# Kernel optimization log

Measured on AMD Instinct MI355X. Metric: run time of the kernel, lower is better.

## Reference

```python
import jax, jax.numpy as jnp
import numpy as np

N_NODES = 20000
EPS_BN = 1e-5
NEG_SLOPE = 0.2


def gat_conv(x, W, att_src, att_dst, bias, src, dst, heads, out_ch, concat):
    n = x.shape[0]
    h = (x @ W).reshape(n, heads, out_ch)                       # [N,H,C]
    a_src = jnp.sum(h * att_src, axis=-1)                       # [N,H]
    a_dst = jnp.sum(h * att_dst, axis=-1)                       # [N,H]
    e = jax.nn.leaky_relu(a_src[src] + a_dst[dst], NEG_SLOPE)   # [E,H]
    # segment softmax over incoming edges of each destination node
    m = jax.ops.segment_max(e, dst, num_segments=n)             # [N,H]
    e = jnp.exp(e - m[dst])
    denom = jax.ops.segment_sum(e, dst, num_segments=n)         # [N,H]
    alpha = e / (denom[dst] + 1e-16)                            # [E,H]
    msg = alpha[:, :, None] * h[src]                            # [E,H,C]
    out = jax.ops.segment_sum(msg, dst, num_segments=n)         # [N,H,C]
    if concat:
        out = out.reshape(n, heads * out_ch)
    else:
        out = out.mean(axis=1)
    return out + bias


def batch_norm(x, gamma, beta):
    mu = x.mean(axis=0)
    var = x.var(axis=0)  # biased, matches torch normalization
    return (x - mu) * jax.lax.rsqrt(var + EPS_BN) * gamma + beta


def setup_inputs() -> dict:
    key = jax.random.key(0)
    ks = jax.random.split(key, 16)
    n, d_in, hid, heads = N_NODES, 768, 128, 8
    n_edges = 160000
    x = jax.random.normal(ks[0], (n, d_in), dtype=jnp.float32)
    edge_index = jax.random.randint(ks[1], (2, n_edges), 0, n, dtype=jnp.int64)
    s = lambda fi, fo: (2.0 / (fi + fo)) ** 0.5
    return {
        "x": x,
        "edge_index": edge_index,
        "W1": jax.random.normal(ks[2], (d_in, heads * hid), jnp.float32) * s(d_in, heads * hid),
        "att_src1": jax.random.normal(ks[3], (heads, hid), jnp.float32) * 0.1,
        "att_dst1": jax.random.normal(ks[4], (heads, hid), jnp.float32) * 0.1,
        "bias1": jnp.zeros((heads * hid,), jnp.float32),
        "bn1_g": jnp.ones((heads * hid,), jnp.float32),
        "bn1_b": jnp.zeros((heads * hid,), jnp.float32),
        "W2": jax.random.normal(ks[5], (heads * hid, hid), jnp.float32) * s(heads * hid, hid),
        "att_src2": jax.random.normal(ks[6], (1, hid), jnp.float32) * 0.1,
        "att_dst2": jax.random.normal(ks[7], (1, hid), jnp.float32) * 0.1,
        "bias2": jnp.zeros((hid,), jnp.float32),
        "bn2_g": jnp.ones((hid,), jnp.float32),
        "bn2_b": jnp.zeros((hid,), jnp.float32),
        "Wc1": jax.random.normal(ks[8], (hid, 64), jnp.float32) * s(hid, 64),
        "bc1": jnp.zeros((64,), jnp.float32),
        "Wc2": jax.random.normal(ks[9], (64, 2), jnp.float32) * s(64, 2),
        "bc2": jnp.zeros((2,), jnp.float32),
    }


def reference(x, edge_index, W1, att_src1, att_dst1, bias1, bn1_g, bn1_b,
              W2, att_src2, att_dst2, bias2, bn2_g, bn2_b,
              Wc1, bc1, Wc2, bc2):
    n = x.shape[0]
    # PyG GATConv default: add self-loops
    loops = jnp.arange(n, dtype=edge_index.dtype)
    src = jnp.concatenate([edge_index[0], loops])
    dst = jnp.concatenate([edge_index[1], loops])

    h = gat_conv(x, W1, att_src1, att_dst1, bias1, src, dst, heads=8, out_ch=128, concat=True)
    h = jax.nn.elu(batch_norm(h, bn1_g, bn1_b))
    # dropout disabled (deterministic reference)
    h = gat_conv(h, W2, att_src2, att_dst2, bias2, src, dst, heads=1, out_ch=128, concat=False)
    h = jax.nn.elu(batch_norm(h, bn2_g, bn2_b))
    h = jax.nn.elu(h @ Wc1 + bc1)
    return h @ Wc2 + bc2  # [N, 2] logits
```

## Files before the change

kernel.cpp:

```cpp
#include <hip/hip_runtime.h>
#include <stdint.h>

typedef unsigned short u16;
typedef __bf16 bf16x8 __attribute__((ext_vector_type(8)));
typedef float f32x4 __attribute__((ext_vector_type(4)));

__device__ __forceinline__ float b2f(u16 u) {
    unsigned x = ((unsigned)u) << 16;
    return __builtin_bit_cast(float, x);
}
__device__ __forceinline__ u16 f2b(float f) {
    unsigned x = __builtin_bit_cast(unsigned, f);
    x = x + 0x7fffu + ((x >> 16) & 1u);
    return (u16)(x >> 16);
}
__device__ __forceinline__ float leaky(float v) { return v > 0.f ? v : 0.2f * v; }
__device__ __forceinline__ float elu(float v) { return v > 0.f ? v : expm1f(v); }

__device__ __forceinline__ void gload16(const u16* g, u16* l) {
    __builtin_amdgcn_global_load_lds((const __attribute__((address_space(1))) void*)(const void*)g,
                                     (__attribute__((address_space(3))) void*)(void*)l, 16, 0, 0);
}

__global__ void k_pre(const float* __restrict__ x, u16* __restrict__ xb,
                      const float* __restrict__ W1, u16* __restrict__ w1t,
                      const float* __restrict__ W2, u16* __restrict__ w2t,
                      const int* __restrict__ ei, int* __restrict__ flag,
                      int* __restrict__ deg, size_t n4, int E0, int N) {
    int bid = blockIdx.x, t = threadIdx.x;
    if (bid < 2048) {
        size_t i = (size_t)bid * 256 + t;
        const size_t stride = (size_t)2048 * 256;
        for (size_t k = i; k < n4; k += stride) {
            float4 v = ((const float4*)x)[k];
            ushort4 o;
            o.x = f2b(v.x); o.y = f2b(v.y); o.z = f2b(v.z); o.w = f2b(v.w);
            ((ushort4*)xb)[k] = o;
        }
        for (size_t k = i; k < (size_t)N; k += stride) deg[k] = 0;
        if (bid == 0) {
            if (t == 0) *flag = 0;
            __syncthreads();
            int lim = E0 < 4096 ? E0 : 4096;
            int any = 0;
            for (int k = t; k < lim; k += 256) any |= (ei[2 * k + 1] != 0);
            if (any) atomicOr(flag, 1);
        }
    } else {
        __shared__ float tile[32][33];
        int b = bid - 2048;
        const float* in; u16* outp; int R, C, cx, ry;
        if (b < 768) { in = W1; outp = w1t; R = 768; C = 1024; cx = b & 31; ry = b >> 5; }
        else { int b2 = b - 768; in = W2; outp = w2t; R = 1024; C = 128; cx = b2 & 3; ry = b2 >> 2; }
        int tx = t & 31, ty = t >> 5;
        int c0 = cx * 32, r0 = ry * 32;
        #pragma unroll
        for (int i = 0; i < 32; i += 8)
            tile[ty + i][tx] = in[(size_t)(r0 + ty + i) * C + c0 + tx];
        __syncthreads();
        #pragma unroll
        for (int i = 0; i < 32; i += 8)
            outp[(size_t)(c0 + ty + i) * R + r0 + tx] = f2b(tile[tx][ty + i]);
    }
}

#define GBM 128
#define GBN 128
#define GBK 64
#define LDT 72
#define SPLITK 4

__global__ __launch_bounds__(256) void k_gemm(const u16* __restrict__ A, const u16* __restrict__ Bt,
                                              u16* __restrict__ C, int M, int NN, int K, int nCB) {
    __shared__ __align__(16) u16 As[GBM][GBK];
    __shared__ __align__(16) u16 Bs[GBN][GBK];
    int nwg = gridDim.x, orig = blockIdx.x;
    int q = nwg >> 3, r8 = nwg & 7, xcd = orig & 7, sub = orig >> 3;
    int wgid = (xcd < r8 ? xcd * (q + 1) : r8 * (q + 1) + (xcd - r8) * q) + sub;
    int rb = wgid / nCB, cb = wgid % nCB;
    int brow = rb * GBM, bcol = cb * GBN;

    int t = threadIdx.x, lane = t & 63, wid = t >> 6;
    int wm = (wid >> 1) * 64, wn = (wid & 1) * 64;
    int fr = lane & 15, fq = lane >> 4;
    f32x4 acc[4][4] = {};
    int srow = lane >> 3;
    int scol = (((lane & 7) ^ srow)) * 8;
    int dcol = (lane & 7) * 8;
    int nK = K / GBK;
    for (int kt = 0; kt < nK; ++kt) {
        int k0 = kt * GBK;
        #pragma unroll
        for (int cc = 0; cc < 8; ++cc) {
            int c = wid * 8 + cc;
            int r = (c & 15) * 8 + srow;
            if (c < 16) gload16(A + (size_t)(brow + r) * K + k0 + scol, &As[r][dcol]);
            else        gload16(Bt + (size_t)(bcol + r) * K + k0 + scol, &Bs[r][dcol]);
        }
        __syncthreads();
        #pragma unroll
        for (int kk = 0; kk < 2; ++kk) {
            int ko = kk * 32 + fq * 8;
            int kos = ko ^ ((fr & 7) << 3);
            bf16x8 af[4], bg[4];
            #pragma unroll
            for (int i = 0; i < 4; ++i) {
                af[i] = *reinterpret_cast<const bf16x8*>(&As[wm + i * 16 + fr][kos]);
                bg[i] = *reinterpret_cast<const bf16x8*>(&Bs[wn + i * 16 + fr][kos]);
            }
            #pragma unroll
            for (int mi = 0; mi < 4; ++mi)
                #pragma unroll
                for (int ni = 0; ni < 4; ++ni)
                    acc[mi][ni] = __builtin_amdgcn_mfma_f32_16x16x32_bf16(af[mi], bg[ni], acc[mi][ni], 0, 0, 0);
        }
        __syncthreads();
    }
    #pragma unroll
    for (int mi = 0; mi < 4; ++mi) {
        #pragma unroll
        for (int j = 0; j < 4; ++j) {
            int row = brow + wm + mi * 16 + fq * 4 + j;
            if (row < M) {
                #pragma unroll
                for (int ni = 0; ni < 4; ++ni) {
                    int col = bcol + wn + ni * 16 + fr;
                    C[(size_t)row * NN + col] = f2b(acc[mi][ni][j]);
                }
            }
        }
    }
}

__global__ __launch_bounds__(256) void k_gemm2(const u16* __restrict__ A, const u16* __restrict__ Bt,
                                               float* __restrict__ Cp, int M, int K,
                                               const float* __restrict__ scA, const float* __restrict__ shA) {
    __shared__ __align__(16) u16 As[GBM][LDT];
    __shared__ __align__(16) u16 Bs[GBN][LDT];
    int brow = blockIdx.x * GBM;
    int ks = blockIdx.y;
    int kBase = ks * (K / SPLITK);
    int t = threadIdx.x;
    int lane = t & 63, wid = t >> 6;
    int wm = (wid >> 1) * 64, wn = (wid & 1) * 64;
    int fr = lane & 15, fq = lane >> 4;
    f32x4 acc[4][4] = {};
    int tr = t >> 3, tc = (t & 7) * 8;
    const int nK = 1024 / SPLITK / GBK;
    for (int kt = 0; kt < nK; ++kt) {
        int k0 = kBase + kt * GBK;
        #pragma unroll
        for (int rr = 0; rr < 4; ++rr) {
            int r = tr + rr * 32;
            int grow = brow + r;
            uint4 bv = *reinterpret_cast<const uint4*>(Bt + (size_t)r * K + k0 + tc);
            *reinterpret_cast<uint4*>(&Bs[r][tc]) = bv;
            uint4 av = make_uint4(0, 0, 0, 0);
            if (grow < M) {
                uint4 u = *reinterpret_cast<const uint4*>(A + (size_t)grow * K + k0 + tc);
                float4 s0 = *(const float4*)(scA + k0 + tc);
                float4 s1 = *(const float4*)(scA + k0 + tc + 4);
                float4 h0 = *(const float4*)(shA + k0 + tc);
                float4 h1 = *(const float4*)(shA + k0 + tc + 4);
                u16 w0 = f2b(elu(b2f((u16)(u.x & 0xffff)) * s0.x + h0.x));
                u16 w1 = f2b(elu(b2f((u16)(u.x >> 16))    * s0.y + h0.y));
                u16 w2 = f2b(elu(b2f((u16)(u.y & 0xffff)) * s0.z + h0.z));
                u16 w3 = f2b(elu(b2f((u16)(u.y >> 16))    * s0.w + h0.w));
                u16 w4 = f2b(elu(b2f((u16)(u.z & 0xffff)) * s1.x + h1.x));
                u16 w5 = f2b(elu(b2f((u16)(u.z >> 16))    * s1.y + h1.y));
                u16 w6 = f2b(elu(b2f((u16)(u.w & 0xffff)) * s1.z + h1.z));
                u16 w7 = f2b(elu(b2f((u16)(u.w >> 16))    * s1.w + h1.w));
                av.x = (unsigned)w0 | ((unsigned)w1 << 16);
                av.y = (unsigned)w2 | ((unsigned)w3 << 16);
                av.z = (unsigned)w4 | ((unsigned)w5 << 16);
                av.w = (unsigned)w6 | ((unsigned)w7 << 16);
            }
            *reinterpret_cast<uint4*>(&As[r][tc]) = av;
        }
        __syncthreads();
        #pragma unroll
        for (int kk = 0; kk < 2; ++kk) {
            int ko = kk * 32 + fq * 8;
            bf16x8 af[4], bg[4];
            #pragma unroll
            for (int i = 0; i < 4; ++i) {
                af[i] = *reinterpret_cast<const bf16x8*>(&As[wm + i * 16 + fr][ko]);
                bg[i] = *reinterpret_cast<const bf16x8*>(&Bs[wn + i * 16 + fr][ko]);
            }
            #pragma unroll
            for (int mi = 0; mi < 4; ++mi)
                #pragma unroll
                for (int ni = 0; ni < 4; ++ni)
                    acc[mi][ni] = __builtin_amdgcn_mfma_f32_16x16x32_bf16(af[mi], bg[ni], acc[mi][ni], 0, 0, 0);
        }
        __syncthreads();
    }
    float* base = Cp + (size_t)ks * M * 128;
    #pragma unroll
    for (int mi = 0; mi < 4; ++mi) {
        #pragma unroll
        for (int j = 0; j < 4; ++j) {
            int row = brow + wm + mi * 16 + fq * 4 + j;
            if (row < M) {
                #pragma unroll
                for (int ni = 0; ni < 4; ++ni) {
                    int col = wn + ni * 16 + fr;
                    base[(size_t)row * 128 + col] = acc[mi][ni][j];
                }
            }
        }
    }
}

__global__ __launch_bounds__(256) void k_red2(const float* __restrict__ Cp,
                                              const float* __restrict__ attS, const float* __restrict__ attD,
                                              u16* __restrict__ h2b, float* __restrict__ asrc,
                                              float* __restrict__ adst, int M) {
    int t = threadIdx.x, lane = t & 63, wid = t >> 6;
    int row = blockIdx.x * 4 + wid;
    if (row >= M) return;
    int c = lane * 2;
    float s0 = 0.f, s1 = 0.f;
    #pragma unroll
    for (int s = 0; s < SPLITK; ++s) {
        float2 v = *(const float2*)(Cp + ((size_t)s * M + row) * 128 + c);
        s0 += v.x; s1 += v.y;
    }
    ushort2 o; o.x = f2b(s0); o.y = f2b(s1);
    *(ushort2*)(h2b + (size_t)row * 128 + c) = o;
    float ps = s0 * attS[c] + s1 * attS[c + 1];
    float pd = s0 * attD[c] + s1 * attD[c + 1];
    #pragma unroll
    for (int m = 1; m < 64; m <<= 1) { ps += __shfl_xor(ps, m); pd += __shfl_xor(pd, m); }
    if (lane == 0) { asrc[row] = ps; adst[row] = pd; }
}

__global__ void k_att8(const u16* __restrict__ h, const float* __restrict__ attS,
                       const float* __restrict__ attD, float* __restrict__ asrc,
                       float* __restrict__ adst, int N) {
    int t = threadIdx.x;
    int half = t >> 7, i = t & 127;
    int row = blockIdx.x * 2 + half;
    if (row >= N) return;
    int head = i >> 4, g = i & 15;
    const u16* hp = h + (size_t)row * 1024 + head * 128 + g * 8;
    const float* sp = attS + head * 128 + g * 8;
    const float* dp = attD + head * 128 + g * 8;
    ushort4 u0 = *(const ushort4*)hp;
    ushort4 u1 = *(const ushort4*)(hp + 4);
    float hv[8] = {b2f(u0.x), b2f(u0.y), b2f(u0.z), b2f(u0.w),
                   b2f(u1.x), b2f(u1.y), b2f(u1.z), b2f(u1.w)};
    float ps = 0.f, pd = 0.f;
    #pragma unroll
    for (int j = 0; j < 8; ++j) { ps += hv[j] * sp[j]; pd += hv[j] * dp[j]; }
    #pragma unroll
    for (int m = 1; m < 16; m <<= 1) { ps += __shfl_xor(ps, m); pd += __shfl_xor(pd, m); }
    if (g == 0) { asrc[row * 8 + head] = ps; adst[row * 8 + head] = pd; }
}

__global__ void k_deg(const int* __restrict__ ei, const int* __restrict__ flag,
                      int* __restrict__ deg, int E0, int E) {
    bool i64 = (*flag == 0);
    for (int e = blockIdx.x * blockDim.x + threadIdx.x; e < E; e += gridDim.x * blockDim.x) {
        int d;
        if (e < E0) d = i64 ? ei[2 * (E0 + e)] : ei[E0 + e];
        else d = e - E0;
        atomicAdd(&deg[d], 1);
    }
}

__global__ __launch_bounds__(1024) void k_scan(const int* __restrict__ deg, int* __restrict__ off,
                                               int* __restrict__ cursor, int n) {
    __shared__ int part[1024];
    int t = threadIdx.x;
    int chunk = (n + 1023) >> 10;
    int beg = t * chunk, end = beg + chunk;
    if (end > n) end = n;
    int s = 0;
    for (int i = beg; i < end; ++i) s += deg[i];
    part[t] = s;
    __syncthreads();
    for (int d = 1; d < 1024; d <<= 1) {
        int v = (t >= d) ? part[t - d] : 0;
        __syncthreads();
        part[t] += v;
        __syncthreads();
    }
    int run = (t == 0) ? 0 : part[t - 1];
    for (int i = beg; i < end; ++i) { off[i] = run; cursor[i] = run; run += deg[i]; }
    if (t == 1023) off[n] = part[1023];
}

__global__ void k_scatter(const int* __restrict__ ei, const int* __restrict__ flag,
                          int* __restrict__ cursor, int* __restrict__ csr, int E0, int E) {
    bool i64 = (*flag == 0);
    for (int e = blockIdx.x * blockDim.x + threadIdx.x; e < E; e += gridDim.x * blockDim.x) {
        int s, d;
        if (e < E0) {
            if (i64) { s = ei[2 * e]; d = ei[2 * (E0 + e)]; }
            else     { s = ei[e];     d = ei[E0 + e]; }
        } else { s = d = e - E0; }
        int pos = atomicAdd(&cursor[d], 1);
        csr[pos] = s;
    }
}

__global__ __launch_bounds__(256) void k_agg1(const int* __restrict__ off, const int* __restrict__ csr,
                                              const float* __restrict__ asrc, const float* __restrict__ adst,
                                              const u16* __restrict__ h1, u16* __restrict__ outg, int N) {
    __shared__ float pch[64][8];
    __shared__ float invs[8];
    int node = blockIdx.x;
    if (node >= N) return;
    int t = threadIdx.x, lane = t & 63, wid = t >> 6;
    int hh = t >> 5;
    int c0 = t * 4;
    int lo = off[node], hi = off[node + 1];
    float ad_l = 0.f, mmax = -1e30f, ssum = 0.f;
    int h = lane & 7, es = lane >> 3;
    if (wid == 0) {
        ad_l = adst[(size_t)node * 8 + h];
        for (int i = lo + es; i < hi; i += 8)
            mmax = fmaxf(mmax, leaky(asrc[(size_t)csr[i] * 8 + h] + ad_l));
        #pragma unroll
        for (int mask = 8; mask < 64; mask <<= 1) mmax = fmaxf(mmax, __shfl_xor(mmax, mask));
    }
    float a0 = 0.f, a1 = 0.f, a2 = 0.f, a3 = 0.f;
    for (int base = lo; base < hi; base += 64) {
        int cend = base + 64 < hi ? base + 64 : hi;
        if (wid == 0) {
            for (int i = base + es; i < cend; i += 8) {
                float p = __expf(leaky(asrc[(size_t)csr[i] * 8 + h] + ad_l) - mmax);
                pch[i - base][h] = p;
                ssum += p;
            }
        }
        __syncthreads();
        for (int i = base; i < cend; ++i) {
            float p = pch[i - base][hh];
            ushort4 u = *(const ushort4*)(h1 + (size_t)csr[i] * 1024 + c0);
            a0 += p * b2f(u.x); a1 += p * b2f(u.y);
            a2 += p * b2f(u.z); a3 += p * b2f(u.w);
        }
        __syncthreads();
    }
    if (wid == 0) {
        #pragma unroll
        for (int mask = 8; mask < 64; mask <<= 1) ssum += __shfl_xor(ssum, mask);
        if (lane < 8) invs[lane] = 1.f / (ssum + 1e-16f);
    }
    __syncthreads();
    float inv = invs[hh];
    ushort4 o;
    o.x = f2b(a0 * inv); o.y = f2b(a1 * inv); o.z = f2b(a2 * inv); o.w = f2b(a3 * inv);
    *(ushort4*)(outg + (size_t)node * 1024 + c0) = o;
}

__global__ __launch_bounds__(128) void k_agg2(const int* __restrict__ off, const int* __restrict__ csr,
                                              const float* __restrict__ asrc, const float* __restrict__ adst,
                                              const u16* __restrict__ h2, u16* __restrict__ outg, int N) {
    __shared__ float pch[64];
    __shared__ float invsh;
    int node = blockIdx.x;
    if (node >= N) return;
    int t = threadIdx.x, lane = t & 63, wid = t >> 6;
    int lo = off[node], hi = off[node + 1];
    float ad = adst[node];
    float mmax = -1e30f, ssum = 0.f;
    if (wid == 0) {
        for (int i = lo + lane; i < hi; i += 64)
            mmax = fmaxf(mmax, leaky(asrc[csr[i]] + ad));
        #pragma unroll
        for (int mask = 1; mask < 64; mask <<= 1) mmax = fmaxf(mmax, __shfl_xor(mmax, mask));
    }
    float acc = 0.f;
    for (int base = lo; base < hi; base += 64) {
        int cend = base + 64 < hi ? base + 64 : hi;
        if (wid == 0 && base + lane < cend) {
            float p = __expf(leaky(asrc[csr[base + lane]] + ad) - mmax);
            pch[lane] = p;
            ssum += p;
        }
        __syncthreads();
        for (int i = base; i < cend; ++i)
            acc += pch[i - base] * b2f(h2[(size_t)csr[i] * 128 + t]);
        __syncthreads();
    }
    if (wid == 0) {
        #pragma unroll
        for (int mask = 1; mask < 64; mask <<= 1) ssum += __shfl_xor(ssum, mask);
        if (lane == 0) invsh = 1.f / (ssum + 1e-16f);
    }
    __syncthreads();
    outg[(size_t)node * 128 + t] = f2b(acc * invsh);
}

template <int CH>
__global__ __launch_bounds__(256) void k_bnpart(const u16* __restrict__ g, float* __restrict__ ps,
                                                float* __restrict__ ps2, int Nrows, int rowsPerChunk) {
    const int TPR = CH / 4;
    const int RPI = 256 / TPR;
    int t = threadIdx.x;
    int rl = t / TPR, c4 = (t % TPR) * 4;
    int chunk = blockIdx.x;
    int r0 = chunk * rowsPerChunk;
    int r1 = r0 + rowsPerChunk; if (r1 > Nrows) r1 = Nrows;
    float s[4] = {0.f, 0.f, 0.f, 0.f}, s2[4] = {0.f, 0.f, 0.f, 0.f};
    for (int r = r0 + rl; r < r1; r += RPI) {
        ushort4 u = *(const ushort4*)(g + (size_t)r * CH + c4);
        float v0 = b2f(u.x), v1 = b2f(u.y), v2 = b2f(u.z), v3 = b2f(u.w);
        s[0] += v0; s2[0] += v0 * v0;
        s[1] += v1; s2[1] += v1 * v1;
        s[2] += v2; s2[2] += v2 * v2;
        s[3] += v3; s2[3] += v3 * v3;
    }
    size_t prow = (size_t)(chunk * RPI + rl) * CH + c4;
    *(float4*)(ps + prow)  = make_float4(s[0], s[1], s[2], s[3]);
    *(float4*)(ps2 + prow) = make_float4(s2[0], s2[1], s2[2], s2[3]);
}

__global__ __launch_bounds__(256) void k_bnfinal(const float* __restrict__ ps, const float* __restrict__ ps2,
                                                 const float* __restrict__ gamma, const float* __restrict__ beta,
                                                 float* __restrict__ scale, float* __restrict__ shift,
                                                 int P, int CH, int Nrows) {
    int t = threadIdx.x, lane = t & 63, wid = t >> 6;
    int col = blockIdx.x * 4 + wid;
    if (col >= CH) return;
    float s = 0.f, s2 = 0.f;
    for (int p = lane; p < P; p += 64) {
        s += ps[(size_t)p * CH + col];
        s2 += ps2[(size_t)p * CH + col];
    }
    #pragma unroll
    for (int m = 1; m < 64; m <<= 1) { s += __shfl_xor(s, m); s2 += __shfl_xor(s2, m); }
    if (lane == 0) {
        double mu = (double)s / Nrows;
        double var = (double)s2 / Nrows - mu * mu;
        if (var < 0) var = 0;
        float sc = gamma[col] * rsqrtf((float)var + 1e-5f);
        scale[col] = sc;
        shift[col] = beta[col] - (float)mu * sc;
    }
}

__global__ __launch_bounds__(256) void k_cls(const u16* __restrict__ g2raw,
                                             const float* __restrict__ scale2, const float* __restrict__ shift2,
                                             const float* __restrict__ Wc1, const float* __restrict__ bc1,
                                             const float* __restrict__ Wc2, const float* __restrict__ bc2,
                                             float* __restrict__ out, int N) {
    __shared__ float wl[128 * 64];
    __shared__ float hs[4][128];
    int t = threadIdx.x, lane = t & 63, wid = t >> 6;
    for (int i = t; i < 128 * 64; i += 256) wl[i] = Wc1[i];
    float sc0 = scale2[2 * lane], sc1 = scale2[2 * lane + 1];
    float sh0 = shift2[2 * lane], sh1 = shift2[2 * lane + 1];
    float bb = bc1[lane];
    float c2a = Wc2[lane * 2], c2b = Wc2[lane * 2 + 1];
    float o2a = bc2[0], o2b = bc2[1];
    __syncthreads();
    int row0 = blockIdx.x * 64;
    for (int it = 0; it < 16; ++it) {
        int row = row0 + it * 4 + wid;
        if (row >= N) continue;
        const u16* hp = g2raw + (size_t)row * 128 + 2 * lane;
        float y0 = b2f(hp[0]) * sc0 + sh0; y0 = y0 > 0.f ? y0 : expm1f(y0);
        float y1 = b2f(hp[1]) * sc1 + sh1; y1 = y1 > 0.f ? y1 : expm1f(y1);
        hs[wid][2 * lane] = y0;
        hs[wid][2 * lane + 1] = y1;
        float tj = bb;
        #pragma unroll 8
        for (int c = 0; c < 128; ++c) tj += hs[wid][c] * wl[c * 64 + lane];
        tj = tj > 0.f ? tj : expm1f(tj);
        float v0 = tj * c2a, v1 = tj * c2b;
        #pragma unroll
        for (int m = 1; m < 64; m <<= 1) { v0 += __shfl_xor(v0, m); v1 += __shfl_xor(v1, m); }
        if (lane == 0) {
            out[(size_t)row * 2 + 0] = v0 + o2a;
            out[(size_t)row * 2 + 1] = v1 + o2b;
        }
    }
}

extern "C" void kernel_launch(void* const* d_in, const int* in_sizes, int n_in,
                              void* d_out, int out_size, void* d_ws, size_t ws_size,
                              hipStream_t stream) {
    const float* x     = (const float*)d_in[0];
    const int*   ei    = (const int*)d_in[1];
    const float* W1    = (const float*)d_in[2];
    const float* attS1 = (const float*)d_in[3];
    const float* attD1 = (const float*)d_in[4];
    const float* bn1g  = (const float*)d_in[6];
    const float* bn1b  = (const float*)d_in[7];
    const float* W2    = (const float*)d_in[8];
    const float* attS2 = (const float*)d_in[9];
    const float* attD2 = (const float*)d_in[10];
    const float* bn2g  = (const float*)d_in[12];
    const float* bn2b  = (const float*)d_in[13];
    const float* Wc1   = (const float*)d_in[14];
    const float* bc1   = (const float*)d_in[15];
    const float* Wc2   = (const float*)d_in[16];
    const float* bc2   = (const float*)d_in[17];
    float* out = (float*)d_out;

    const int DIN = 768, F1 = 1024, C2 = 128;
    int N = in_sizes[0] / DIN;
    int E0 = in_sizes[1] / 2;
    int E = E0 + N;
    const int nMB = (N + GBM - 1) / GBM;
    const int Mp = nMB * GBM;

    char* w = (char*)d_ws;
    auto take = [&](size_t bytes) -> void* {
        void* p = (void*)w;
        w += (bytes + 255) & ~(size_t)255;
        return p;
    };
    u16* xb     = (u16*)take((size_t)Mp * DIN * 2);
    u16* bufA   = (u16*)take((size_t)N * F1 * 2);
    u16* h1b    = (u16*)take((size_t)N * F1 * 2);
    u16* w1t    = (u16*)take((size_t)F1 * DIN * 2);
    u16* w2t    = (u16*)take((size_t)C2 * F1 * 2);
    float* asrc1 = (float*)take((size_t)N * 8 * 4);
    float* adst1 = (float*)take((size_t)N * 8 * 4);
    int* deg    = (int*)take((size_t)N * 4);
    int* off    = (int*)take((size_t)(N + 1) * 4);
    int* cursor = (int*)take((size_t)N * 4);
    int* csr    = (int*)take((size_t)E * 4);
    int* flag   = (int*)take(256);
    u16* h2b    = (u16*)take((size_t)N * C2 * 2);
    float* asrc2 = (float*)take((size_t)N * 4);
    float* adst2 = (float*)take((size_t)N * 4);
    u16* g2     = (u16*)take((size_t)N * C2 * 2);
    float* scale1 = (float*)take(F1 * 4);
    float* shift1 = (float*)take(F1 * 4);
    float* scale2 = (float*)take(C2 * 4);
    float* shift2 = (float*)take(C2 * 4);
    float* psA   = (float*)take((size_t)1024 * 1024 * 4);
    float* psB   = (float*)take((size_t)1024 * 1024 * 4);
    float* part  = (float*)h1b;

    size_t n4 = (size_t)N * DIN / 4;

    k_pre<<<2048 + 896, 256, 0, stream>>>(x, xb, W1, w1t, W2, w2t, ei, flag, deg, n4, E0, N);

    k_gemm<<<nMB * (F1 / GBN), 256, 0, stream>>>(xb, w1t, h1b, N, F1, DIN, F1 / GBN);
    k_att8<<<(N + 1) / 2, 256, 0, stream>>>(h1b, attS1, attD1, asrc1, adst1, N);

    k_deg<<<512, 256, 0, stream>>>(ei, flag, deg, E0, E);
    k_scan<<<1, 1024, 0, stream>>>(deg, off, cursor, N);
    k_scatter<<<512, 256, 0, stream>>>(ei, flag, cursor, csr, E0, E);

    k_agg1<<<N, 256, 0, stream>>>(off, csr, asrc1, adst1, h1b, bufA, N);
    {
        int nchunk = 256, rpc = (N + nchunk - 1) / nchunk;
        k_bnpart<1024><<<nchunk, 256, 0, stream>>>(bufA, psA, psB, N, rpc);
        k_bnfinal<<<F1 / 4, 256, 0, stream>>>(psA, psB, bn1g, bn1b, scale1, shift1, nchunk, F1, N);
    }

    k_gemm2<<<dim3(nMB, SPLITK), 256, 0, stream>>>(bufA, w2t, part, N, F1, scale1, shift1);
    k_red2<<<(N + 3) / 4, 256, 0, stream>>>(part, attS2, attD2, h2b, asrc2, adst2, N);

    k_agg2<<<N, 128, 0, stream>>>(off, csr, asrc2, adst2, h2b, g2, N);
    {
        int nchunk = 128, rpc = (N + nchunk - 1) / nchunk;
        k_bnpart<128><<<nchunk, 256, 0, stream>>>(g2, psA, psB, N, rpc);
        k_bnfinal<<<C2 / 4, 256, 0, stream>>>(psA, psB, bn2g, bn2b, scale2, shift2, nchunk * 8, C2, N);
    }

    k_cls<<<(N + 63) / 64, 256, 0, stream>>>(g2, scale2, shift2, Wc1, bc1, Wc2, bc2, out, N);
}
```

Before: 340.7 us.

## Merge attention-score and degree kernels; split agg1 edge loop across two thread halves

The per-node attention-score kernel and the degree-count kernel become one launch, with block index choosing which work a block does. This removes one launch and lets the two independent jobs overlap. In the first-layer aggregation, each thread now loads 8 bf16 channels with a 16-byte load instead of 4. The two 128-thread halves of the block take alternating edges, and their partial sums are combined through shared memory at the end. The aim is wider memory accesses and more loads in flight per node, at the cost of extra shared memory and a final reduction step.

```diff
diff --git a/kernel.cpp b/kernel.cpp
--- a/kernel.cpp
+++ b/kernel.cpp
@@ -235,37 +235,39 @@
     if (lane == 0) { asrc[row] = ps; adst[row] = pd; }
 }
 
-__global__ void k_att8(const u16* __restrict__ h, const float* __restrict__ attS,
-                       const float* __restrict__ attD, float* __restrict__ asrc,
-                       float* __restrict__ adst, int N) {
-    int t = threadIdx.x;
-    int half = t >> 7, i = t & 127;
-    int row = blockIdx.x * 2 + half;
-    if (row >= N) return;
-    int head = i >> 4, g = i & 15;
-    const u16* hp = h + (size_t)row * 1024 + head * 128 + g * 8;
-    const float* sp = attS + head * 128 + g * 8;
-    const float* dp = attD + head * 128 + g * 8;
-    ushort4 u0 = *(const ushort4*)hp;
-    ushort4 u1 = *(const ushort4*)(hp + 4);
-    float hv[8] = {b2f(u0.x), b2f(u0.y), b2f(u0.z), b2f(u0.w),
-                   b2f(u1.x), b2f(u1.y), b2f(u1.z), b2f(u1.w)};
-    float ps = 0.f, pd = 0.f;
-    #pragma unroll
-    for (int j = 0; j < 8; ++j) { ps += hv[j] * sp[j]; pd += hv[j] * dp[j]; }
-    #pragma unroll
-    for (int m = 1; m < 16; m <<= 1) { ps += __shfl_xor(ps, m); pd += __shfl_xor(pd, m); }
-    if (g == 0) { asrc[row * 8 + head] = ps; adst[row * 8 + head] = pd; }
-}
-
-__global__ void k_deg(const int* __restrict__ ei, const int* __restrict__ flag,
-                      int* __restrict__ deg, int E0, int E) {
-    bool i64 = (*flag == 0);
-    for (int e = blockIdx.x * blockDim.x + threadIdx.x; e < E; e += gridDim.x * blockDim.x) {
-        int d;
-        if (e < E0) d = i64 ? ei[2 * (E0 + e)] : ei[E0 + e];
-        else d = e - E0;
-        atomicAdd(&deg[d], 1);
+__global__ void k_attdeg(const u16* __restrict__ h, const float* __restrict__ attS,
+                         const float* __restrict__ attD, float* __restrict__ asrc,
+                         float* __restrict__ adst, const int* __restrict__ ei,
+                         const int* __restrict__ flag, int* __restrict__ deg,
+                         int N, int E0, int E, int nAtt) {
+    int bid = blockIdx.x, t = threadIdx.x;
+    if (bid < nAtt) {
+        int half = t >> 7, i = t & 127;
+        int row = bid * 2 + half;
+        if (row >= N) return;
+        int head = i >> 4, g = i & 15;
+        const u16* hp = h + (size_t)row * 1024 + head * 128 + g * 8;
+        const float* sp = attS + head * 128 + g * 8;
+        const float* dp = attD + head * 128 + g * 8;
+        ushort4 u0 = *(const ushort4*)hp;
+        ushort4 u1 = *(const ushort4*)(hp + 4);
+        float hv[8] = {b2f(u0.x), b2f(u0.y), b2f(u0.z), b2f(u0.w),
+                       b2f(u1.x), b2f(u1.y), b2f(u1.z), b2f(u1.w)};
+        float ps = 0.f, pd = 0.f;
+        #pragma unroll
+        for (int j = 0; j < 8; ++j) { ps += hv[j] * sp[j]; pd += hv[j] * dp[j]; }
+        #pragma unroll
+        for (int m = 1; m < 16; m <<= 1) { ps += __shfl_xor(ps, m); pd += __shfl_xor(pd, m); }
+        if (g == 0) { asrc[row * 8 + head] = ps; adst[row * 8 + head] = pd; }
+    } else {
+        int b = bid - nAtt;
+        bool i64 = (*flag == 0);
+        for (int e = b * 256 + t; e < E; e += 512 * 256) {
+            int d;
+            if (e < E0) d = i64 ? ei[2 * (E0 + e)] : ei[E0 + e];
+            else d = e - E0;
+            atomicAdd(&deg[d], 1);
+        }
     }
 }
 
@@ -310,11 +312,13 @@
                                               const u16* __restrict__ h1, u16* __restrict__ outg, int N) {
     __shared__ float pch[64][8];
     __shared__ float invs[8];
+    __shared__ float red[128][9];
     int node = blockIdx.x;
     if (node >= N) return;
     int t = threadIdx.x, lane = t & 63, wid = t >> 6;
-    int hh = t >> 5;
-    int c0 = t * 4;
+    int tl = t & 127, te = t >> 7;
+    int hh = tl >> 4;
+    int c0 = tl * 8;
     int lo = off[node], hi = off[node + 1];
     float ad_l = 0.f, mmax = -1e30f, ssum = 0.f;
     int h = lane & 7, es = lane >> 3;
@@ -325,7 +329,7 @@
         #pragma unroll
         for (int mask = 8; mask < 64; mask <<= 1) mmax = fmaxf(mmax, __shfl_xor(mmax, mask));
     }
-    float a0 = 0.f, a1 = 0.f, a2 = 0.f, a3 = 0.f;
+    float a[8] = {};
     for (int base = lo; base < hi; base += 64) {
         int cend = base + 64 < hi ? base + 64 : hi;
         if (wid == 0) {
@@ -336,11 +340,17 @@
             }
         }
         __syncthreads();
-        for (int i = base; i < cend; ++i) {
+        for (int i = base + te; i < cend; i += 2) {
             float p = pch[i - base][hh];
-            ushort4 u = *(const ushort4*)(h1 + (size_t)csr[i] * 1024 + c0);
-            a0 += p * b2f(u.x); a1 += p * b2f(u.y);
-            a2 += p * b2f(u.z); a3 += p * b2f(u.w);
+            uint4 u = *(const uint4*)(h1 + (size_t)csr[i] * 1024 + c0);
+            a[0] += p * b2f((u16)(u.x & 0xffff));
+            a[1] += p * b2f((u16)(u.x >> 16));
+            a[2] += p * b2f((u16)(u.y & 0xffff));
+            a[3] += p * b2f((u16)(u.y >> 16));
+            a[4] += p * b2f((u16)(u.z & 0xffff));
+            a[5] += p * b2f((u16)(u.z >> 16));
+            a[6] += p * b2f((u16)(u.w & 0xffff));
+            a[7] += p * b2f((u16)(u.w >> 16));
         }
         __syncthreads();
     }
@@ -349,11 +359,22 @@
         for (int mask = 8; mask < 64; mask <<= 1) ssum += __shfl_xor(ssum, mask);
         if (lane < 8) invs[lane] = 1.f / (ssum + 1e-16f);
     }
+    if (te == 1) {
+        #pragma unroll
+        for (int j = 0; j < 8; ++j) red[tl][j] = a[j];
+    }
     __syncthreads();
-    float inv = invs[hh];
-    ushort4 o;
-    o.x = f2b(a0 * inv); o.y = f2b(a1 * inv); o.z = f2b(a2 * inv); o.w = f2b(a3 * inv);
-    *(ushort4*)(outg + (size_t)node * 1024 + c0) = o;
+    if (te == 0) {
+        float inv = invs[hh];
+        #pragma unroll
+        for (int j = 0; j < 8; ++j) a[j] = (a[j] + red[tl][j]) * inv;
+        uint4 o;
+        o.x = (unsigned)f2b(a[0]) | ((unsigned)f2b(a[1]) << 16);
+        o.y = (unsigned)f2b(a[2]) | ((unsigned)f2b(a[3]) << 16);
+        o.z = (unsigned)f2b(a[4]) | ((unsigned)f2b(a[5]) << 16);
+        o.w = (unsigned)f2b(a[6]) | ((unsigned)f2b(a[7]) << 16);
+        *(uint4*)(outg + (size_t)node * 1024 + c0) = o;
+    }
 }
 
 __global__ __launch_bounds__(128) void k_agg2(const int* __restrict__ off, const int* __restrict__ csr,
@@ -540,13 +561,13 @@
     float* part  = (float*)h1b;
 
     size_t n4 = (size_t)N * DIN / 4;
+    int nAtt = (N + 1) / 2;
 
     k_pre<<<2048 + 896, 256, 0, stream>>>(x, xb, W1, w1t, W2, w2t, ei, flag, deg, n4, E0, N);
 
     k_gemm<<<nMB * (F1 / GBN), 256, 0, stream>>>(xb, w1t, h1b, N, F1, DIN, F1 / GBN);
-    k_att8<<<(N + 1) / 2, 256, 0, stream>>>(h1b, attS1, attD1, asrc1, adst1, N);
-
-    k_deg<<<512, 256, 0, stream>>>(ei, flag, deg, E0, E);
+    k_attdeg<<<nAtt + 512, 256, 0, stream>>>(h1b, attS1, attD1, asrc1, adst1, ei, flag, deg, N, E0, E, nAtt);
+
     k_scan<<<1, 1024, 0, stream>>>(deg, off, cursor, N);
     k_scatter<<<512, 256, 0, stream>>>(ei, flag, cursor, csr, E0, E);
 
```

New measurement: 337.4 us, median of 2. Within noise of the previous version (-1.0%).
